# Kernel tuning notes

Measured on AMD Instinct MI355X. Metric: run time of the kernel, lower is better.

## Reference

```python
import jax, jax.numpy as jnp
import numpy as np
import math

EMBED_DIM = 768
NUM_FRAMES = 48
NUM_FREQS = 10
C_IN = 3
FOURIER_DIM = 4 * NUM_FREQS  # include_uv=False
PM_HID = C_IN * 9 * 4        # patch_mlp_ratio=4
OM_HID = EMBED_DIM * 4       # out_mlp_ratio=4
B, N, T, H, W = 4, 8192, 48, 256, 256


def setup_inputs() -> dict:
    key = jax.random.key(0)
    ks = jax.random.split(key, 16)
    uv = jax.random.uniform(ks[0], (B, N, 2), dtype=jnp.float32)
    ts = jax.random.randint(ks[1], (B, N, 3), 0, NUM_FRAMES).astype(jnp.float32)
    query = jnp.concatenate([uv, ts], axis=-1)  # (B,N,5)
    images = jax.random.normal(ks[2], (B, C_IN, T, H, W), dtype=jnp.float32)
    def xavier(k, fan_in, fan_out):
        lim = math.sqrt(6.0 / (fan_in + fan_out))
        return jax.random.uniform(k, (fan_in, fan_out), dtype=jnp.float32, minval=-lim, maxval=lim)
    return {
        "query": query,
        "images": images,
        "uv_w": xavier(ks[3], FOURIER_DIM, EMBED_DIM),
        "uv_b": jnp.zeros((EMBED_DIM,), jnp.float32),
        "t_src_emb": 0.02 * jax.random.normal(ks[4], (NUM_FRAMES, EMBED_DIM), dtype=jnp.float32),
        "t_tgt_emb": 0.02 * jax.random.normal(ks[5], (NUM_FRAMES, EMBED_DIM), dtype=jnp.float32),
        "t_cam_emb": 0.02 * jax.random.normal(ks[6], (NUM_FRAMES, EMBED_DIM), dtype=jnp.float32),
        "pm_w1": xavier(ks[7], C_IN * 9, PM_HID),
        "pm_b1": jnp.zeros((PM_HID,), jnp.float32),
        "pm_w2": xavier(ks[8], PM_HID, EMBED_DIM),
        "pm_b2": jnp.zeros((EMBED_DIM,), jnp.float32),
        "om_w1": xavier(ks[9], EMBED_DIM, OM_HID),
        "om_b1": jnp.zeros((OM_HID,), jnp.float32),
        "om_w2": xavier(ks[10], OM_HID, EMBED_DIM),
        "om_b2": jnp.zeros((EMBED_DIM,), jnp.float32),
    }


def reference(query, images, uv_w, uv_b, t_src_emb, t_tgt_emb, t_cam_emb,
              pm_w1, pm_b1, pm_w2, pm_b2, om_w1, om_b1, om_w2, om_b2):
    # images: (B,C,T,H,W) -> (B,T,C,H,W)
    images = jnp.transpose(images, (0, 2, 1, 3, 4))
    Bq, Nq, _ = query.shape
    _, Tq, C, Hh, Ww = images.shape

    uv = jnp.clip(query[..., 0:2].astype(jnp.float32), 0.0, 1.0)  # (B,N,2)
    t_src = jnp.clip(jnp.round(query[..., 2]).astype(jnp.int32), 0, NUM_FRAMES - 1)
    t_tgt = jnp.clip(jnp.round(query[..., 3]).astype(jnp.int32), 0, NUM_FRAMES - 1)
    t_cam = jnp.clip(jnp.round(query[..., 4]).astype(jnp.int32), 0, NUM_FRAMES - 1)

    # Fourier features of (u,v)
    fb = 2.0 ** jnp.arange(NUM_FREQS, dtype=jnp.float32)  # (F,)
    u = uv[..., 0:1]
    v = uv[..., 1:2]
    up = (2.0 * math.pi) * u * fb  # (B,N,F)
    vp = (2.0 * math.pi) * v * fb
    feat = jnp.concatenate([jnp.sin(up), jnp.cos(up), jnp.sin(vp), jnp.cos(vp)], axis=-1)

    token1 = feat @ uv_w + uv_b              # (B,N,D)
    token2 = t_src_emb[t_src]                # embedding lookups
    token3 = t_tgt_emb[t_tgt]
    token4 = t_cam_emb[t_cam]

    # 3x3 patch gather centered at discrete (u,v) pixel of frame t_src
    x = jnp.round(uv[..., 0] * (Ww - 1)).astype(jnp.int32)  # (B,N)
    y = jnp.round(uv[..., 1] * (Hh - 1)).astype(jnp.int32)
    d = jnp.arange(-1, 2, dtype=jnp.int32)
    x_idx = jnp.clip(x[..., None] + d, 0, Ww - 1)  # (B,N,3)
    y_idx = jnp.clip(y[..., None] + d, 0, Hh - 1)  # (B,N,3)
    b_idx = jnp.arange(Bq)[:, None, None, None, None]
    c_idx = jnp.arange(C)[:, None, None]
    # direct fancy-index gather -> (B,N,C,3,3); avoids materializing (B,N,C,H,W)
    patches = images[b_idx,
                     t_src[:, :, None, None, None],
                     c_idx,
                     y_idx[:, :, None, :, None],
                     x_idx[:, :, None, None, :]]
    patch_flat = patches.reshape(Bq, Nq, C * 9)

    h = jax.nn.gelu(patch_flat @ pm_w1 + pm_b1, approximate=False)
    token5 = h @ pm_w2 + pm_b2

    out = token1 + token2 + token3 + token4 + token5
    out = jax.nn.gelu(out @ om_w1 + om_b1, approximate=False) @ om_w2 + om_b2
    return out
```

## Files before the change

kernel.cpp:

```cpp
#include <hip/hip_runtime.h>

typedef __bf16 bf16x8 __attribute__((ext_vector_type(8)));
typedef float  f32x4  __attribute__((ext_vector_type(4)));

#define GAS(p) ((const __attribute__((address_space(1))) void*)(p))
#define LAS(p) ((__attribute__((address_space(3))) void*)(p))

__device__ __forceinline__ float gelu_exact(float x) {
    return 0.5f * x * (1.f + erff(x * 0.70710678118654752440f));
}

__global__ __launch_bounds__(256) void stage1_kernel(
    const float* __restrict__ query, const float* __restrict__ images,
    const float* __restrict__ pm_w1, const float* __restrict__ pm_b1,
    __bf16* __restrict__ G, int* __restrict__ tbuf)
{
    __shared__ float patch[4][28];
    const int wave = threadIdx.x >> 6, lane = threadIdx.x & 63;
    const int p = blockIdx.x * 4 + wave;
    const float* q = query + (size_t)p * 5;
    float u = fminf(fmaxf(q[0], 0.f), 1.f);
    float v = fminf(fmaxf(q[1], 0.f), 1.f);
    int ts = min(max((int)rintf(q[2]), 0), 47);
    int tt = min(max((int)rintf(q[3]), 0), 47);
    int tc = min(max((int)rintf(q[4]), 0), 47);
    const int b = p >> 13;
    if (lane < 27) {
        int c = lane / 9, rem = lane % 9, dy = rem / 3, dx = rem % 3;
        int x = (int)rintf(u * 255.f), y = (int)rintf(v * 255.f);
        int xx = min(max(x + dx - 1, 0), 255);
        int yy = min(max(y + dy - 1, 0), 255);
        size_t idx = ((size_t)((b * 3 + c) * 48 + ts) << 16) + ((size_t)yy << 8) + (size_t)xx;
        patch[wave][lane] = images[idx];
    }
    if (lane < 40) {
        int i = lane % 10;
        float base = (lane < 20) ? u : v;
        float ph = 6.28318530717958647693f * base * exp2f((float)i);
        float val = ((lane / 10) & 1) ? cosf(ph) : sinf(ph);
        G[(size_t)p * 192 + lane] = (__bf16)val;
    }
    for (int j = 148 + lane; j < 192; j += 64) G[(size_t)p * 192 + j] = (__bf16)0.f;
    if (lane < 3) tbuf[p * 3 + lane] = (lane == 0) ? ts : (lane == 1) ? tt : tc;
    __syncthreads();
    for (int j = lane; j < 108; j += 64) {
        float acc = pm_b1[j];
        #pragma unroll
        for (int i2 = 0; i2 < 27; i2++)
            acc = fmaf(patch[wave][i2], pm_w1[i2 * 108 + j], acc);
        G[(size_t)p * 192 + 40 + j] = (__bf16)gelu_exact(acc);
    }
}

__global__ __launch_bounds__(256) void transpose_to_bf16(
    const float* __restrict__ src, __bf16* __restrict__ dst, int R, int C)
{
    __shared__ float t[32][33];
    const int c0 = blockIdx.x * 32, r0 = blockIdx.y * 32;
    const int tx = threadIdx.x & 31, ty = threadIdx.x >> 5;
    #pragma unroll
    for (int i = 0; i < 32; i += 8)
        t[ty + i][tx] = src[(size_t)(r0 + ty + i) * C + (c0 + tx)];
    __syncthreads();
    #pragma unroll
    for (int i = 0; i < 32; i += 8)
        dst[(size_t)(c0 + ty + i) * R + (r0 + tx)] = (__bf16)t[tx][ty + i];
}

__global__ __launch_bounds__(256) void build_wcat(
    const float* __restrict__ uv_w, const float* __restrict__ pm_w2, __bf16* __restrict__ Wt)
{
    int idx = blockIdx.x * 256 + threadIdx.x;
    int n = idx / 192, k = idx % 192;
    float v = 0.f;
    if (k < 40) v = uv_w[k * 768 + n];
    else if (k < 148) v = pm_w2[(k - 40) * 768 + n];
    Wt[idx] = (__bf16)v;
}

enum { EPI_X = 0, EPI_GELU = 1, EPI_OUT = 2 };

template <int EPI, typename OutT>
__global__ __launch_bounds__(256) void gemm_bt(
    const __bf16* __restrict__ A, const __bf16* __restrict__ Bt, int K,
    const float* __restrict__ bias, const float* __restrict__ bias2,
    const int* __restrict__ tbuf,
    const float* __restrict__ e0, const float* __restrict__ e1, const float* __restrict__ e2,
    OutT* __restrict__ Cmat, int N)
{
    __shared__ __attribute__((aligned(16))) __bf16 As[128 * 64];
    __shared__ __attribute__((aligned(16))) __bf16 Bs[128 * 64];
    const int tid = threadIdx.x;
    const int wave = tid >> 6, lane = tid & 63;
    const int wr = wave >> 1, wc = wave & 1;
    const int quad = lane >> 4, l15 = lane & 15;
    const int sw = l15 & 7;

    const int ntiles = N >> 7;
    const int per_super = ntiles << 3;
    const int id = blockIdx.x;
    const int sup = id / per_super, rem = id - sup * per_super;
    const long m0 = (long)(sup * 8 + (rem & 7)) << 7;
    const long n0 = (long)(rem >> 3) << 7;

    f32x4 acc[4][4];
    #pragma unroll
    for (int i = 0; i < 4; i++)
        #pragma unroll
        for (int j = 0; j < 4; j++)
            #pragma unroll
            for (int r = 0; r < 4; r++)
                acc[i][j][r] = 0.f;

    const __bf16* pa[4]; const __bf16* pb[4];
    __bf16* la[4]; __bf16* lb[4];
    #pragma unroll
    for (int t = 0; t < 4; t++) {
        int c = (t * 4 + wave) * 64 + lane;
        int row = c >> 3, s = c & 7, g = s ^ (row & 7);
        pa[t] = A  + (m0 + row) * (long)K + g * 8;
        pb[t] = Bt + (n0 + row) * (long)K + g * 8;
        la[t] = As + (t * 4 + wave) * 512;
        lb[t] = Bs + (t * 4 + wave) * 512;
    }

    for (int kt = 0; kt < K; kt += 64) {
        #pragma unroll
        for (int t = 0; t < 4; t++) {
            __builtin_amdgcn_global_load_lds(GAS(pa[t] + kt), LAS(la[t]), 16, 0, 0);
            __builtin_amdgcn_global_load_lds(GAS(pb[t] + kt), LAS(lb[t]), 16, 0, 0);
        }
        __syncthreads();
        #pragma unroll
        for (int h = 0; h < 2; h++) {
            const int slot = ((h * 4 + quad) ^ sw) * 8;
            bf16x8 af[4], bfv[4];
            #pragma unroll
            for (int i = 0; i < 4; i++)
                af[i] = *(const bf16x8*)&As[(wr * 64 + i * 16 + l15) * 64 + slot];
            #pragma unroll
            for (int j = 0; j < 4; j++)
                bfv[j] = *(const bf16x8*)&Bs[(wc * 64 + j * 16 + l15) * 64 + slot];
            #pragma unroll
            for (int i = 0; i < 4; i++)
                #pragma unroll
                for (int j = 0; j < 4; j++)
                    acc[i][j] = __builtin_amdgcn_mfma_f32_16x16x32_bf16(af[i], bfv[j], acc[i][j], 0, 0, 0);
        }
        __syncthreads();
    }

    #pragma unroll
    for (int i = 0; i < 4; i++) {
        #pragma unroll
        for (int r = 0; r < 4; r++) {
            long row = m0 + wr * 64 + i * 16 + quad * 4 + r;
            int t0 = 0, t1 = 0, t2 = 0;
            if constexpr (EPI == EPI_X) {
                t0 = tbuf[row * 3 + 0];
                t1 = tbuf[row * 3 + 1];
                t2 = tbuf[row * 3 + 2];
            }
            #pragma unroll
            for (int j = 0; j < 4; j++) {
                long col = n0 + wc * 64 + j * 16 + l15;
                float val = acc[i][j][r];
                if constexpr (EPI == EPI_X) {
                    val += bias[col] + bias2[col];
                    val += e0[t0 * 768 + col] + e1[t1 * 768 + col] + e2[t2 * 768 + col];
                    Cmat[row * (long)N + col] = (OutT)val;
                } else if constexpr (EPI == EPI_GELU) {
                    val += bias[col];
                    Cmat[row * (long)N + col] = (OutT)gelu_exact(val);
                } else {
                    val += bias[col];
                    Cmat[row * (long)N + col] = (OutT)val;
                }
            }
        }
    }
}

static constexpr size_t OFF_G  = 0;
static constexpr size_t OFF_T  = 12582912;
static constexpr size_t OFF_WC = 12976128;
static constexpr size_t OFF_W1 = 13271040;
static constexpr size_t OFF_W2 = 17989632;
static constexpr size_t OFF_X  = 22708224;
static constexpr size_t OFF_H2 = 73039872;

extern "C" void kernel_launch(void* const* d_in, const int* in_sizes, int n_in,
                              void* d_out, int out_size, void* d_ws, size_t ws_size,
                              hipStream_t stream)
{
    const float* query  = (const float*)d_in[0];
    const float* images = (const float*)d_in[1];
    const float* uv_w   = (const float*)d_in[2];
    const float* uv_b   = (const float*)d_in[3];
    const float* e_src  = (const float*)d_in[4];
    const float* e_tgt  = (const float*)d_in[5];
    const float* e_cam  = (const float*)d_in[6];
    const float* pm_w1  = (const float*)d_in[7];
    const float* pm_b1  = (const float*)d_in[8];
    const float* pm_w2  = (const float*)d_in[9];
    const float* pm_b2  = (const float*)d_in[10];
    const float* om_w1  = (const float*)d_in[11];
    const float* om_b1  = (const float*)d_in[12];
    const float* om_w2  = (const float*)d_in[13];
    const float* om_b2  = (const float*)d_in[14];
    float* out = (float*)d_out;
    char* ws = (char*)d_ws;

    __bf16* G    = (__bf16*)(ws + OFF_G);
    int*    tb   = (int*)(ws + OFF_T);
    __bf16* Wcat = (__bf16*)(ws + OFF_WC);
    __bf16* W1t  = (__bf16*)(ws + OFF_W1);
    __bf16* W2t  = (__bf16*)(ws + OFF_W2);
    __bf16* X    = (__bf16*)(ws + OFF_X);
    __bf16* H2   = (__bf16*)(ws + OFF_H2);

    stage1_kernel<<<8192, 256, 0, stream>>>(query, images, pm_w1, pm_b1, G, tb);
    transpose_to_bf16<<<dim3(3072 / 32, 768 / 32), 256, 0, stream>>>(om_w1, W1t, 768, 3072);
    transpose_to_bf16<<<dim3(768 / 32, 3072 / 32), 256, 0, stream>>>(om_w2, W2t, 3072, 768);
    build_wcat<<<576, 256, 0, stream>>>(uv_w, pm_w2, Wcat);

    gemm_bt<EPI_X, __bf16><<<256 * 6, 256, 0, stream>>>(
        G, Wcat, 192, uv_b, pm_b2, tb, e_src, e_tgt, e_cam, X, 768);

    long Mc = 1024;
    for (long cand = 32768; cand >= 1024; cand >>= 1)
        if (OFF_H2 + (size_t)cand * 3072 * 2 <= ws_size) { Mc = cand; break; }

    for (long m = 0; m < 32768; m += Mc) {
        gemm_bt<EPI_GELU, __bf16><<<(Mc / 128) * 24, 256, 0, stream>>>(
            X + m * 768, W1t, 768, om_b1, nullptr, nullptr, nullptr, nullptr, nullptr, H2, 3072);
        gemm_bt<EPI_OUT, float><<<(Mc / 128) * 6, 256, 0, stream>>>(
            H2, W2t, 3072, om_b2, nullptr, nullptr, nullptr, nullptr, nullptr, out + m * 768, 768);
    }
}
```

Measured before the change: 711.3 us.

## Add 256x256-tile 512-thread GEMM with 4-stage LDS pipeline for output MLP

Introduces a new gemm256 kernel with 256x256 output tiles, 8 waves, and a 4-deep global_load_lds ring buffer using explicit vmcnt waits, then uses it for the two large output-MLP GEMMs. Larger tiles raise arithmetic intensity and data reuse, and the deeper prefetch is meant to hide memory latency. The cost is 128KB of dynamic LDS per block and a large accumulator register footprint, which may cap occupancy. With 256-row tiles the M=32768 GEMMs get fewer blocks, which may hurt wave balance across CUs.

```diff
diff --git a/kernel.cpp b/kernel.cpp
--- a/kernel.cpp
+++ b/kernel.cpp
@@ -5,10 +5,13 @@
 
 #define GAS(p) ((const __attribute__((address_space(1))) void*)(p))
 #define LAS(p) ((__attribute__((address_space(3))) void*)(p))
+#define VMCNT(n) asm volatile("s_waitcnt vmcnt(" #n ")" ::: "memory")
 
 __device__ __forceinline__ float gelu_exact(float x) {
     return 0.5f * x * (1.f + erff(x * 0.70710678118654752440f));
 }
+
+enum { EPI_X = 0, EPI_GELU = 1, EPI_OUT = 2 };
 
 __global__ __launch_bounds__(256) void stage1_kernel(
     const float* __restrict__ query, const float* __restrict__ images,
@@ -78,8 +81,6 @@
     Wt[idx] = (__bf16)v;
 }
 
-enum { EPI_X = 0, EPI_GELU = 1, EPI_OUT = 2 };
-
 template <int EPI, typename OutT>
 __global__ __launch_bounds__(256) void gemm_bt(
     const __bf16* __restrict__ A, const __bf16* __restrict__ Bt, int K,
@@ -176,6 +177,118 @@
                     val += bias[col];
                     Cmat[row * (long)N + col] = (OutT)val;
                 }
+            }
+        }
+    }
+}
+
+template <int EPI, typename OutT>
+__global__ __launch_bounds__(512, 2) void gemm256(
+    const __bf16* __restrict__ A, const __bf16* __restrict__ Bt, int K,
+    const float* __restrict__ bias, OutT* __restrict__ Cmat, int N)
+{
+    extern __shared__ __attribute__((aligned(16))) __bf16 smem[];
+    const int tid = threadIdx.x;
+    const int wave = tid >> 6, lane = tid & 63;
+    const int wr = wave >> 2, wc = wave & 3;
+    const int quad = lane >> 4, l15 = lane & 15;
+
+    const int ntiles = N >> 8;
+    const int per_super = ntiles << 3;
+    const int id = blockIdx.x;
+    const int sup = id / per_super, rem = id - sup * per_super;
+    const long m0 = (long)(sup * 8 + (rem & 7)) << 8;
+    const long n0 = (long)(rem >> 3) << 8;
+
+    f32x4 acc[8][4];
+    #pragma unroll
+    for (int i = 0; i < 8; i++)
+        #pragma unroll
+        for (int n = 0; n < 4; n++)
+            #pragma unroll
+            for (int r = 0; r < 4; r++)
+                acc[i][n][r] = 0.f;
+
+    const __bf16* srcA[2]; const __bf16* srcB[2];
+    int ldsA[2], ldsB[2];
+    #pragma unroll
+    for (int i = 0; i < 2; i++) {
+        int c = i * 512 + tid;
+        int row = c >> 2, s = c & 3, g = s ^ ((row >> 1) & 3);
+        srcA[i] = A  + (m0 + row) * (long)K + g * 8;
+        srcB[i] = Bt + (n0 + row) * (long)K + g * 8;
+        ldsA[i] = (i * 512 + wave * 64) * 8;
+        ldsB[i] = (i * 512 + wave * 64) * 8;
+    }
+
+    auto stage = [&](int t) {
+        const int buf = (t & 3) * 8192;
+        const long koff = (long)t * 32;
+        #pragma unroll
+        for (int i = 0; i < 2; i++) {
+            __builtin_amdgcn_global_load_lds(GAS(srcA[i] + koff), LAS(smem + buf + ldsA[i]), 16, 0, 0);
+            __builtin_amdgcn_global_load_lds(GAS(srcB[i] + koff), LAS(smem + 32768 + buf + ldsB[i]), 16, 0, 0);
+        }
+    };
+
+    const int slot = ((quad ^ ((l15 >> 1) & 3)) * 8);
+    const int aoff = (wr * 128 + l15) * 32 + slot;
+    const int boff = (wc * 64 + l15) * 32 + slot;
+
+    auto compute = [&](int j) {
+        const __bf16* ab = smem + (j & 3) * 8192 + aoff;
+        const __bf16* bb = smem + 32768 + (j & 3) * 8192 + boff;
+        bf16x8 af[8], bv[4];
+        #pragma unroll
+        for (int i = 0; i < 8; i++) af[i] = *(const bf16x8*)(ab + i * 512);
+        #pragma unroll
+        for (int n = 0; n < 4; n++) bv[n] = *(const bf16x8*)(bb + n * 512);
+        __builtin_amdgcn_s_setprio(1);
+        #pragma unroll
+        for (int i = 0; i < 8; i++)
+            #pragma unroll
+            for (int n = 0; n < 4; n++)
+                acc[i][n] = __builtin_amdgcn_mfma_f32_16x16x32_bf16(af[i], bv[n], acc[i][n], 0, 0, 0);
+        __builtin_amdgcn_s_setprio(0);
+        __builtin_amdgcn_sched_barrier(0);
+    };
+
+    const int nk = K >> 5;
+    stage(0); stage(1); stage(2);
+    for (int j = 0; j < nk - 3; ++j) {
+        __builtin_amdgcn_s_barrier();
+        stage(j + 3);
+        VMCNT(12);
+        __builtin_amdgcn_s_barrier();
+        __builtin_amdgcn_sched_barrier(0);
+        compute(j);
+    }
+    VMCNT(8);
+    __builtin_amdgcn_s_barrier();
+    __builtin_amdgcn_sched_barrier(0);
+    compute(nk - 3);
+    VMCNT(4);
+    __builtin_amdgcn_s_barrier();
+    __builtin_amdgcn_sched_barrier(0);
+    compute(nk - 2);
+    VMCNT(0);
+    __builtin_amdgcn_s_barrier();
+    __builtin_amdgcn_sched_barrier(0);
+    compute(nk - 1);
+
+    #pragma unroll
+    for (int i = 0; i < 8; i++) {
+        #pragma unroll
+        for (int r = 0; r < 4; r++) {
+            const long row = m0 + wr * 128 + i * 16 + quad * 4 + r;
+            #pragma unroll
+            for (int n = 0; n < 4; n++) {
+                const long col = n0 + wc * 64 + n * 16 + l15;
+                float val = acc[i][n][r] + bias[col];
+                if constexpr (EPI == EPI_GELU)
+                    Cmat[row * (long)N + col] = (OutT)gelu_exact(val);
+                else
+                    Cmat[row * (long)N + col] = (OutT)val;
             }
         }
     }
@@ -219,6 +332,15 @@
     __bf16* X    = (__bf16*)(ws + OFF_X);
     __bf16* H2   = (__bf16*)(ws + OFF_H2);
 
+    static bool attr_done = false;
+    if (!attr_done) {
+        hipFuncSetAttribute(reinterpret_cast<const void*>(gemm256<EPI_GELU, __bf16>),
+                            hipFuncAttributeMaxDynamicSharedMemorySize, 131072);
+        hipFuncSetAttribute(reinterpret_cast<const void*>(gemm256<EPI_OUT, float>),
+                            hipFuncAttributeMaxDynamicSharedMemorySize, 131072);
+        attr_done = true;
+    }
+
     stage1_kernel<<<8192, 256, 0, stream>>>(query, images, pm_w1, pm_b1, G, tb);
     transpose_to_bf16<<<dim3(3072 / 32, 768 / 32), 256, 0, stream>>>(om_w1, W1t, 768, 3072);
     transpose_to_bf16<<<dim3(768 / 32, 3072 / 32), 256, 0, stream>>>(om_w2, W2t, 3072, 768);
@@ -232,9 +354,9 @@
         if (OFF_H2 + (size_t)cand * 3072 * 2 <= ws_size) { Mc = cand; break; }
 
     for (long m = 0; m < 32768; m += Mc) {
-        gemm_bt<EPI_GELU, __bf16><<<(Mc / 128) * 24, 256, 0, stream>>>(
-            X + m * 768, W1t, 768, om_b1, nullptr, nullptr, nullptr, nullptr, nullptr, H2, 3072);
-        gemm_bt<EPI_OUT, float><<<(Mc / 128) * 6, 256, 0, stream>>>(
-            H2, W2t, 3072, om_b2, nullptr, nullptr, nullptr, nullptr, nullptr, out + m * 768, 768);
-    }
-}
+        gemm256<EPI_GELU, __bf16><<<(Mc / 256) * 12, 512, 131072, stream>>>(
+            X + m * 768, W1t, 768, om_b1, H2, 3072);
+        gemm256<EPI_OUT, float><<<(Mc / 256) * 3, 512, 131072, stream>>>(
+            H2, W2t, 3072, om_b2, out + m * 768, 768);
+    }
+}
```

Measured after the change: 706.0 us. About the same (-0.7%).
